# Kernel optimization log

Measured on AMD Instinct MI355X. Metric: run time of the kernel, lower is better.

Reference implementation:

```python
import jax, jax.numpy as jnp
import numpy as np
import math

B, T, C, H = 8, 1024, 1024, 16
D = C // H  # head_size = 64
FF = 4 * C


def setup_inputs() -> dict:
    key = jax.random.key(0)
    ks = jax.random.split(key, 8)
    s = 0.02
    return {
        "x": jax.random.normal(ks[0], (B, T, C), jnp.float32),
        "ln1_g": jnp.ones((C,), jnp.float32),
        "ln1_b": jnp.zeros((C,), jnp.float32),
        "attn_w": jax.random.normal(ks[1], (C, 3 * C), jnp.float32) * s,
        "attn_b": jnp.zeros((3 * C,), jnp.float32),
        "attn_proj_w": jax.random.normal(ks[2], (C, C), jnp.float32) * s,
        "attn_proj_b": jnp.zeros((C,), jnp.float32),
        "ln2_g": jnp.ones((C,), jnp.float32),
        "ln2_b": jnp.zeros((C,), jnp.float32),
        "fc_w": jax.random.normal(ks[3], (C, FF), jnp.float32) * s,
        "fc_b": jnp.zeros((FF,), jnp.float32),
        "mlp_proj_w": jax.random.normal(ks[4], (FF, C), jnp.float32) * s,
        "mlp_proj_b": jnp.zeros((C,), jnp.float32),
    }


def _layernorm(x, g, b, eps=1e-5):
    mu = jnp.mean(x, axis=-1, keepdims=True)
    var = jnp.mean(jnp.square(x - mu), axis=-1, keepdims=True)
    return (x - mu) * jax.lax.rsqrt(var + eps) * g + b


def reference(x, ln1_g, ln1_b, attn_w, attn_b, attn_proj_w, attn_proj_b,
              ln2_g, ln2_b, fc_w, fc_b, mlp_proj_w, mlp_proj_b):
    # --- attention branch (pre-LN) ---
    h = _layernorm(x, ln1_g, ln1_b)
    kqv = h @ attn_w + attn_b                      # (B,T,3C)
    # NOTE: source splits as k, q, v (k first!)
    k, q, v = jnp.split(kqv, 3, axis=-1)
    k = k.reshape(B, T, H, D).transpose(0, 2, 1, 3)  # (B,H,T,D)
    q = q.reshape(B, T, H, D).transpose(0, 2, 1, 3)
    v = v.reshape(B, T, H, D).transpose(0, 2, 1, 3)
    # NOTE: source computes k @ q^T, i.e. wei[i,j] = k_i . q_j
    scale = 1.0 / math.sqrt(D)
    wei = jnp.einsum('bhid,bhjd->bhij', k, q) * scale  # (B,H,T,T)
    causal = jnp.tril(jnp.ones((T, T), dtype=bool))
    wei = jnp.where(causal, wei, -jnp.inf)
    wei = jax.nn.softmax(wei, axis=-1)
    out = jnp.einsum('bhij,bhjd->bhid', wei, v)        # (B,H,T,D)
    out = out.transpose(0, 2, 1, 3).reshape(B, T, C)
    out = out @ attn_proj_w + attn_proj_b
    x = x + out
    # --- MLP branch (pre-LN) ---
    h2 = _layernorm(x, ln2_g, ln2_b)
    m = jax.nn.gelu(h2 @ fc_w + fc_b, approximate=False)  # torch GELU default = exact erf
    m = m @ mlp_proj_w + mlp_proj_b
    return x + m
```

## Files before the change

kernel.cpp:

```cpp
#include <hip/hip_runtime.h>
#include <stdint.h>

typedef unsigned short u16;
typedef __bf16 bf16x8 __attribute__((ext_vector_type(8)));
typedef float f32x4 __attribute__((ext_vector_type(4)));

#define DEVINL static __device__ __forceinline__

DEVINL u16 f2bf(float f) {
  uint32_t u = __builtin_bit_cast(uint32_t, f);
  u += 0x7fffu + ((u >> 16) & 1u);
  return (u16)(u >> 16);
}

DEVINL uint32_t pack_bf2(float f0, float f1) {
  uint32_t u0 = __builtin_bit_cast(uint32_t, f0) + 0x8000u;
  uint32_t u1 = __builtin_bit_cast(uint32_t, f1) + 0x8000u;
  return __builtin_amdgcn_perm(u1, u0, 0x07060302u);
}

DEVINL bf16x8 ld_frag(const u16* p) { return *(const bf16x8*)p; }

DEVINL void gld_lds16(const void* g, void* l) {
  __builtin_amdgcn_global_load_lds((const __attribute__((address_space(1))) void*)g,
                                   (__attribute__((address_space(3))) void*)l, 16, 0, 0);
}

DEVINL int swz4(int r) { return (r & 3) ^ ((r >> 2) & 3); }

DEVINL void xcd_tile(int& tm, int& tn) {
  const int gx = gridDim.x;
  const int flat = blockIdx.x + gx * blockIdx.y;
  const int q = (gx * gridDim.y) >> 3;
  const int wg = (flat & 7) * q + (flat >> 3);
  tn = (wg % gx) * 128;
  tm = (wg / gx) * 128;
}

DEVINL void xcd_tile_wide(int& tm, int& tn) {
  const int gx = gridDim.x;
  const int flat = blockIdx.x + gx * blockIdx.y;
  const int q = (gx * gridDim.y) >> 3;
  const int wg = (flat & 7) * q + (flat >> 3);
  tn = (wg % gx) * 128;
  tm = (wg / gx) * 256;
}

__global__ __launch_bounds__(256)
void transpose_bf16(const float* __restrict__ W, u16* __restrict__ Wt, int K, int N) {
  __shared__ float tile[32][33];
  const int n0 = blockIdx.x * 32, k0 = blockIdx.y * 32;
  const int tx = threadIdx.x, ty = threadIdx.y;
#pragma unroll
  for (int i = 0; i < 32; i += 8)
    tile[ty + i][tx] = W[(size_t)(k0 + ty + i) * N + n0 + tx];
  __syncthreads();
#pragma unroll
  for (int i = 0; i < 32; i += 8)
    Wt[(size_t)(n0 + ty + i) * K + k0 + tx] = f2bf(tile[tx][ty + i]);
}

__global__ __launch_bounds__(256)
void ln_kernel(const float* __restrict__ x, const float* __restrict__ g,
               const float* __restrict__ b, u16* __restrict__ out) {
  __shared__ float red[8];
  const size_t row = blockIdx.x;
  const int tid = threadIdx.x;
  float4 v = ((const float4*)(x + row * 1024))[tid];
  float s = v.x + v.y + v.z + v.w;
  float s2 = v.x * v.x + v.y * v.y + v.z * v.z + v.w * v.w;
#pragma unroll
  for (int o = 32; o; o >>= 1) { s += __shfl_down(s, o); s2 += __shfl_down(s2, o); }
  const int w = tid >> 6;
  if ((tid & 63) == 0) { red[w * 2] = s; red[w * 2 + 1] = s2; }
  __syncthreads();
  const float S = red[0] + red[2] + red[4] + red[6];
  const float S2 = red[1] + red[3] + red[5] + red[7];
  const float mu = S * (1.f / 1024.f);
  const float var = S2 * (1.f / 1024.f) - mu * mu;
  const float rstd = rsqrtf(var + 1e-5f);
  float4 gv = ((const float4*)g)[tid];
  float4 bv = ((const float4*)b)[tid];
  ushort4 o;
  o.x = f2bf((v.x - mu) * rstd * gv.x + bv.x);
  o.y = f2bf((v.y - mu) * rstd * gv.y + bv.y);
  o.z = f2bf((v.z - mu) * rstd * gv.z + bv.z);
  o.w = f2bf((v.w - mu) * rstd * gv.w + bv.w);
  ((ushort4*)(out + row * 1024))[tid] = o;
}

enum { EPI_KQV = 0, EPI_RESID = 1, EPI_GELU = 2, EPI_ADD = 3 };

template <int EPI>
DEVINL void gemm_epilogue(f32x4 (&acc)[4][4], const float* __restrict__ bias,
                          void* __restrict__ outp, const float* __restrict__ resid,
                          int N, int tm, int tn, int mh, int nh, int q4, int c) {
#pragma unroll
  for (int mt = 0; mt < 4; ++mt) {
#pragma unroll
    for (int nt = 0; nt < 4; ++nt) {
      const int col = tn + nh + nt * 16 + c;
      const float bcol = bias[col];
#pragma unroll
      for (int rg = 0; rg < 4; ++rg) {
        const int row = tm + mh + mt * 16 + q4 * 4 + rg;
        float val = acc[mt][nt][rg] + bcol;
        if constexpr (EPI == EPI_KQV) {
          const int bb = row >> 10, t = row & 1023;
          const int s = col >> 10, rem = col & 1023;
          const int hh = rem >> 6, d = rem & 63;
          if (s == 0) val *= 0.18033688011112042f;
          const size_t base = ((size_t)((bb * 16 + hh) * 3 + s)) << 16;
          const size_t idx = (s == 2) ? base + (size_t)d * 1024 + t : base + (size_t)t * 64 + d;
          ((u16*)outp)[idx] = f2bf(val);
        } else if constexpr (EPI == EPI_RESID) {
          const size_t idx = (size_t)row * 1024 + col;
          ((float*)outp)[idx] = val + resid[idx];
        } else if constexpr (EPI == EPI_GELU) {
          const float x2 = val * val;
          const float t = __builtin_fmaf(x2, -0.102952445f, -2.30221235f);
          const float e = __builtin_amdgcn_exp2f(val * t);
          const float ge = val * __builtin_amdgcn_rcpf(1.0f + e);
          ((u16*)outp)[(size_t)row * N + col] = f2bf(ge);
        } else {
          const size_t idx = (size_t)row * 1024 + col;
          ((float*)outp)[idx] += val;
        }
      }
    }
  }
}

template <int EPI>
DEVINL void gemm_body2(const u16* __restrict__ A, const u16* __restrict__ Bt,
                       const float* __restrict__ bias, void* __restrict__ outp,
                       const float* __restrict__ resid, int M, int N, int K,
                       int tm, int tn) {
  __shared__ alignas(16) u16 sA[2][128 * 32];
  __shared__ alignas(16) u16 sB[2][128 * 32];
  const int tid = threadIdx.x;
  const int w = tid >> 6, l = tid & 63;
  const int q4 = l >> 4, c = l & 15;
  const int mh = (w >> 1) * 64, nh = (w & 1) * 64;
  const int cg8 = (q4 ^ swz4(c)) * 8;

  f32x4 acc[4][4] = {};

  const int srow = l >> 2;
  const int scol = ((l & 3) ^ swz4(srow)) * 8;
  const u16* gA0 = A + (size_t)(tm + (w * 2) * 16 + srow) * K + scol;
  const u16* gA1 = A + (size_t)(tm + (w * 2 + 1) * 16 + srow) * K + scol;
  const u16* gB0 = Bt + (size_t)(tn + (w * 2) * 16 + srow) * K + scol;
  const u16* gB1 = Bt + (size_t)(tn + (w * 2 + 1) * 16 + srow) * K + scol;
  const int cA0 = (w * 2) * 512, cA1 = (w * 2 + 1) * 512;

  const int nIters = K / 32;
#define STAGE2(buf, k0)                         \
  do {                                          \
    gld_lds16(gA0 + (k0), &sA[buf][cA0]);       \
    gld_lds16(gA1 + (k0), &sA[buf][cA1]);       \
    gld_lds16(gB0 + (k0), &sB[buf][cA0]);       \
    gld_lds16(gB1 + (k0), &sB[buf][cA1]);       \
  } while (0)

  STAGE2(0, 0);
  for (int i = 0; i < nIters; ++i) {
    const int cur = i & 1;
    asm volatile("s_waitcnt vmcnt(0)" ::: "memory");
    __syncthreads();
    if (i + 1 < nIters) STAGE2(cur ^ 1, (i + 1) * 32);
    const u16* bA = sA[cur];
    const u16* bB = sB[cur];
    bf16x8 af[4], bfv[4];
#pragma unroll
    for (int mt = 0; mt < 4; ++mt) af[mt] = ld_frag(bA + (mh + mt * 16 + c) * 32 + cg8);
#pragma unroll
    for (int nt = 0; nt < 4; ++nt) bfv[nt] = ld_frag(bB + (nh + nt * 16 + c) * 32 + cg8);
#pragma unroll
    for (int mt = 0; mt < 4; ++mt)
#pragma unroll
      for (int nt = 0; nt < 4; ++nt)
        acc[mt][nt] = __builtin_amdgcn_mfma_f32_16x16x32_bf16(af[mt], bfv[nt], acc[mt][nt], 0, 0, 0);
  }
#undef STAGE2
  gemm_epilogue<EPI>(acc, bias, outp, resid, N, tm, tn, mh, nh, q4, c);
}

template <int EPI>
DEVINL void gemm_bodyW(const u16* __restrict__ A, const u16* __restrict__ Bt,
                       const float* __restrict__ bias, void* __restrict__ outp,
                       const float* __restrict__ resid, int N, int K,
                       int tm, int tn) {
  __shared__ alignas(16) u16 sT[3][48 * 512];
  const int tid = threadIdx.x;
  const int w = tid >> 6, l = tid & 63;
  const int q4 = l >> 4, c = l & 15;
  const int mh = (w >> 1) * 64, nh = (w & 1) * 64;

  f32x4 acc[4][4] = {};

  const int lr = l >> 3;
  const int lc = ((l & 7) ^ lr) * 8;
  const u16* gA[4];
  const u16* gB[2];
#pragma unroll
  for (int j = 0; j < 4; ++j) gA[j] = A + (size_t)(tm + 32 * w + j * 8 + lr) * K + lc;
#pragma unroll
  for (int j = 0; j < 2; ++j) gB[j] = Bt + (size_t)(tn + 16 * w + j * 8 + lr) * K + lc;

  auto stageW = [&](int buf, int k0) {
#pragma unroll
    for (int j = 0; j < 4; ++j) gld_lds16(gA[j] + k0, &sT[buf][(4 * w + j) * 512]);
#pragma unroll
    for (int j = 0; j < 2; ++j) gld_lds16(gB[j] + k0, &sT[buf][(32 + 2 * w + j) * 512]);
  };

  auto computeW = [&](int cur) {
    const u16* bufA = sT[cur];
    const u16* bufB = sT[cur] + 32 * 512;
#pragma unroll
    for (int kh = 0; kh < 2; ++kh) {
      bf16x8 af[4], bfv[4];
#pragma unroll
      for (int mt = 0; mt < 4; ++mt) {
        const int row = mh + mt * 16 + c;
        af[mt] = ld_frag(bufA + row * 64 + ((kh * 4 + q4) ^ (c & 7)) * 8);
      }
#pragma unroll
      for (int nt = 0; nt < 4; ++nt) {
        const int row = nh + nt * 16 + c;
        bfv[nt] = ld_frag(bufB + row * 64 + ((kh * 4 + q4) ^ (c & 7)) * 8);
      }
      __builtin_amdgcn_s_setprio(1);
#pragma unroll
      for (int mt = 0; mt < 4; ++mt)
#pragma unroll
        for (int nt = 0; nt < 4; ++nt)
          acc[mt][nt] = __builtin_amdgcn_mfma_f32_16x16x32_bf16(af[mt], bfv[nt], acc[mt][nt], 0, 0, 0);
      __builtin_amdgcn_s_setprio(0);
    }
  };

  const int nI = K / 64;
  stageW(0, 0);
  stageW(1, 64);
  int bc = 0;
  int i = 0;
  for (; i < nI - 1; ++i) {
    asm volatile("s_waitcnt vmcnt(6)" ::: "memory");
    __builtin_amdgcn_s_barrier();
    asm volatile("" ::: "memory");
    if (i + 2 < nI) {
      const int tgt = (bc >= 1) ? bc - 1 : 2;
      stageW(tgt, (i + 2) * 64);
    }
    computeW(bc);
    bc = (bc < 2) ? bc + 1 : 0;
  }
  asm volatile("s_waitcnt vmcnt(0)" ::: "memory");
  __builtin_amdgcn_s_barrier();
  asm volatile("" ::: "memory");
  computeW(bc);

  gemm_epilogue<EPI>(acc, bias, outp, resid, N, tm, tn, mh, nh, q4, c);
}

__global__ __launch_bounds__(256)
void gemm_kqv(const u16* __restrict__ A, const u16* __restrict__ Bt,
              const float* __restrict__ bias, u16* __restrict__ outp,
              int M, int N, int K) {
  int tm, tn;
  xcd_tile(tm, tn);
  gemm_body2<EPI_KQV>(A, Bt, bias, outp, nullptr, M, N, K, tm, tn);
}

__global__ __launch_bounds__(512)
void gemm_gelu(const u16* __restrict__ A, const u16* __restrict__ Bt,
               const float* __restrict__ bias, u16* __restrict__ outp,
               int M, int N, int K) {
  int tm, tn;
  xcd_tile_wide(tm, tn);
  gemm_bodyW<EPI_GELU>(A, Bt, bias, outp, nullptr, N, K, tm, tn);
}

__global__ __launch_bounds__(512)
void gemm_resid(const u16* __restrict__ A, const u16* __restrict__ Bt,
                const float* __restrict__ bias, float* __restrict__ outp,
                const float* __restrict__ resid, int M, int N, int K) {
  int tm, tn;
  xcd_tile_wide(tm, tn);
  gemm_bodyW<EPI_RESID>(A, Bt, bias, outp, resid, N, K, tm, tn);
}

__global__ __launch_bounds__(512)
void gemm_add(const u16* __restrict__ A, const u16* __restrict__ Bt,
              const float* __restrict__ bias, float* __restrict__ outp,
              int M, int N, int K) {
  int tm, tn;
  xcd_tile_wide(tm, tn);
  gemm_bodyW<EPI_ADD>(A, Bt, bias, outp, nullptr, N, K, tm, tn);
}

__global__ __launch_bounds__(256)
void attn_kernel(const u16* __restrict__ kqv, u16* __restrict__ outp) {
  constexpr int LS = 72;
  __shared__ alignas(16) u16 sP[64 * LS];
  __shared__ alignas(16) u16 sK[64 * LS];
  __shared__ alignas(16) u16 sV[64 * LS];
  const int bh = blockIdx.x;
  const int it = (int)gridDim.y - 1 - (int)blockIdx.y;
  const int tid = threadIdx.x;
  const int w = tid >> 6, l = tid & 63, q4 = l >> 4, c = l & 15;
  const int il = w * 16 + c;
  const size_t hb = (size_t)bh * 3 * 65536;
  const u16* qbase = kqv + hb;
  const u16* kbase = kqv + hb + 65536;
  const u16* vbase = kqv + hb + 2 * 65536;

  const int sr = tid >> 3, sc = (tid & 7) * 8;
  const int sr2 = sr + 32;
  *(int4*)&sP[sr * LS + sc] = *(const int4*)(qbase + (size_t)(it * 64 + sr) * 64 + sc);
  *(int4*)&sP[sr2 * LS + sc] = *(const int4*)(qbase + (size_t)(it * 64 + sr2) * 64 + sc);

  f32x4 oacc[4] = {};
  float lsum = 0.f;
  bf16x8 bq0, bq1;

  int4 rk0 = *(const int4*)(kbase + (size_t)sr * 64 + sc);
  int4 rk1 = *(const int4*)(kbase + (size_t)sr2 * 64 + sc);
  int4 rv0 = *(const int4*)(vbase + (size_t)sr * 1024 + sc);
  int4 rv1 = *(const int4*)(vbase + (size_t)sr2 * 1024 + sc);

  for (int jt = 0; jt <= it; ++jt) {
    if (jt) __syncthreads();
    *(int4*)&sK[sr * LS + sc] = rk0;
    *(int4*)&sK[sr2 * LS + sc] = rk1;
    *(int4*)&sV[sr * LS + sc] = rv0;
    *(int4*)&sV[sr2 * LS + sc] = rv1;
    __syncthreads();
    if (jt < it) {
      rk0 = *(const int4*)(kbase + (size_t)((jt + 1) * 64 + sr) * 64 + sc);
      rk1 = *(const int4*)(kbase + (size_t)((jt + 1) * 64 + sr2) * 64 + sc);
      rv0 = *(const int4*)(vbase + (size_t)sr * 1024 + (jt + 1) * 64 + sc);
      rv1 = *(const int4*)(vbase + (size_t)sr2 * 1024 + (jt + 1) * 64 + sc);
    }
    if (jt == 0) {
      bq0 = ld_frag(sP + il * LS + q4 * 8);
      bq1 = ld_frag(sP + il * LS + 32 + q4 * 8);
    }

    f32x4 st[4] = {};
#pragma unroll
    for (int nt = 0; nt < 4; ++nt) {
      st[nt] = __builtin_amdgcn_mfma_f32_16x16x32_bf16(
          ld_frag(sK + (nt * 16 + c) * LS + q4 * 8), bq0, st[nt], 0, 0, 0);
      st[nt] = __builtin_amdgcn_mfma_f32_16x16x32_bf16(
          ld_frag(sK + (nt * 16 + c) * LS + 32 + q4 * 8), bq1, st[nt], 0, 0, 0);
    }

    const bool diag = (jt == it);
    u16* prow = sP + il * LS;
#pragma unroll
    for (int nt = 0; nt < 4; ++nt) {
      float e0 = __builtin_amdgcn_exp2f(st[nt][0]);
      float e1 = __builtin_amdgcn_exp2f(st[nt][1]);
      float e2 = __builtin_amdgcn_exp2f(st[nt][2]);
      float e3 = __builtin_amdgcn_exp2f(st[nt][3]);
      if (diag) {
        const int jb = nt * 16 + q4 * 4;
        e0 = (jb + 0 > il) ? 0.f : e0;
        e1 = (jb + 1 > il) ? 0.f : e1;
        e2 = (jb + 2 > il) ? 0.f : e2;
        e3 = (jb + 3 > il) ? 0.f : e3;
      }
      lsum += (e0 + e1) + (e2 + e3);
      uint2 pk = {pack_bf2(e0, e1), pack_bf2(e2, e3)};
      *(uint2*)&prow[nt * 16 + q4 * 4] = pk;
    }

    bf16x8 bp0 = ld_frag(sP + il * LS + q4 * 8);
    bf16x8 bp1 = ld_frag(sP + il * LS + 32 + q4 * 8);
#pragma unroll
    for (int dt = 0; dt < 4; ++dt) {
      oacc[dt] = __builtin_amdgcn_mfma_f32_16x16x32_bf16(
          ld_frag(sV + (dt * 16 + c) * LS + q4 * 8), bp0, oacc[dt], 0, 0, 0);
      oacc[dt] = __builtin_amdgcn_mfma_f32_16x16x32_bf16(
          ld_frag(sV + (dt * 16 + c) * LS + 32 + q4 * 8), bp1, oacc[dt], 0, 0, 0);
    }
  }

  lsum += __shfl_xor(lsum, 16);
  lsum += __shfl_xor(lsum, 32);
  const float linv = 1.f / lsum;

  const int b_ = bh >> 4, h_ = bh & 15;
  const int t_ = it * 64 + il;
  u16* orow = outp + ((size_t)(b_ * 1024 + t_)) * 1024 + h_ * 64;
#pragma unroll
  for (int dt = 0; dt < 4; ++dt) {
    uint2 ok = {pack_bf2(oacc[dt][0] * linv, oacc[dt][1] * linv),
                pack_bf2(oacc[dt][2] * linv, oacc[dt][3] * linv)};
    *(uint2*)&orow[dt * 16 + q4 * 4] = ok;
  }
}

extern "C" void kernel_launch(void* const* d_in, const int* in_sizes, int n_in,
                              void* d_out, int out_size, void* d_ws, size_t ws_size,
                              hipStream_t stream) {
  const float* x       = (const float*)d_in[0];
  const float* ln1_g   = (const float*)d_in[1];
  const float* ln1_b   = (const float*)d_in[2];
  const float* attn_w  = (const float*)d_in[3];
  const float* attn_b  = (const float*)d_in[4];
  const float* attn_pw = (const float*)d_in[5];
  const float* attn_pb = (const float*)d_in[6];
  const float* ln2_g   = (const float*)d_in[7];
  const float* ln2_b   = (const float*)d_in[8];
  const float* fc_w    = (const float*)d_in[9];
  const float* fc_b    = (const float*)d_in[10];
  const float* mlp_w   = (const float*)d_in[11];
  const float* mlp_b   = (const float*)d_in[12];
  float* out = (float*)d_out;

  u16* ws = (u16*)d_ws;
  u16* mlpT     = ws;
  u16* attn_wT  = mlpT + 1024 * 4096;
  u16* attn_pwT = attn_wT + 3072 * 1024;
  u16* fcT      = attn_pwT + 1024 * 1024;
  u16* hbuf     = fcT + 4096 * 1024;
  u16* kqv      = hbuf + 8192 * 1024;
  u16* attn_o   = kqv + (size_t)8192 * 3072;
  u16* mbuf     = kqv;

  dim3 tb(32, 8);
  transpose_bf16<<<dim3(96, 32),  tb, 0, stream>>>(attn_w,  attn_wT,  1024, 3072);
  transpose_bf16<<<dim3(32, 32),  tb, 0, stream>>>(attn_pw, attn_pwT, 1024, 1024);
  transpose_bf16<<<dim3(128, 32), tb, 0, stream>>>(fc_w,    fcT,      1024, 4096);
  transpose_bf16<<<dim3(32, 128), tb, 0, stream>>>(mlp_w,   mlpT,     4096, 1024);

  ln_kernel<<<8192, 256, 0, stream>>>(x, ln1_g, ln1_b, hbuf);

  gemm_kqv<<<dim3(24, 64), 256, 0, stream>>>(hbuf, attn_wT, attn_b, kqv, 8192, 3072, 1024);

  attn_kernel<<<dim3(128, 16), 256, 0, stream>>>(kqv, attn_o);

  gemm_resid<<<dim3(8, 32), 512, 0, stream>>>(attn_o, attn_pwT, attn_pb, out, x,
                                              8192, 1024, 1024);

  ln_kernel<<<8192, 256, 0, stream>>>(out, ln2_g, ln2_b, hbuf);

  gemm_gelu<<<dim3(32, 32), 512, 0, stream>>>(hbuf, fcT, fc_b, mbuf, 8192, 4096, 1024);

  gemm_add<<<dim3(8, 32), 512, 0, stream>>>(mbuf, mlpT, mlp_b, out, 8192, 1024, 4096);
}
```

Measured before the change: 468.0 us.

## Enlarge attention query tile to 128 rows with 512-thread blocks, drop register prefetch

The attention kernel now handles 128 query rows per block with 8 waves instead of 64 rows with 4 waves, so each loaded K/V tile is shared by twice as many queries. Waves whose rows lie entirely above a key tile skip that tile's compute, and the causal mask uses a per-row threshold. The register double-buffered prefetch of the next K/V tile is removed, so global loads now sit directly between the barriers. The grid is halved, which lowers parallelism and makes per-block work less even across the causal triangle.

```diff
diff --git a/kernel.cpp b/kernel.cpp
--- a/kernel.cpp
+++ b/kernel.cpp
@@ -301,10 +301,10 @@
   gemm_bodyW<EPI_ADD>(A, Bt, bias, outp, nullptr, N, K, tm, tn);
 }
 
-__global__ __launch_bounds__(256)
+__global__ __launch_bounds__(512)
 void attn_kernel(const u16* __restrict__ kqv, u16* __restrict__ outp) {
   constexpr int LS = 72;
-  __shared__ alignas(16) u16 sP[64 * LS];
+  __shared__ alignas(16) u16 sP[128 * LS];
   __shared__ alignas(16) u16 sK[64 * LS];
   __shared__ alignas(16) u16 sV[64 * LS];
   const int bh = blockIdx.x;
@@ -318,36 +318,26 @@
   const u16* vbase = kqv + hb + 2 * 65536;
 
   const int sr = tid >> 3, sc = (tid & 7) * 8;
-  const int sr2 = sr + 32;
-  *(int4*)&sP[sr * LS + sc] = *(const int4*)(qbase + (size_t)(it * 64 + sr) * 64 + sc);
-  *(int4*)&sP[sr2 * LS + sc] = *(const int4*)(qbase + (size_t)(it * 64 + sr2) * 64 + sc);
+  *(int4*)&sP[sr * LS + sc] = *(const int4*)(qbase + (size_t)(it * 128 + sr) * 64 + sc);
+  *(int4*)&sP[(sr + 64) * LS + sc] =
+      *(const int4*)(qbase + (size_t)(it * 128 + sr + 64) * 64 + sc);
 
   f32x4 oacc[4] = {};
   float lsum = 0.f;
   bf16x8 bq0, bq1;
 
-  int4 rk0 = *(const int4*)(kbase + (size_t)sr * 64 + sc);
-  int4 rk1 = *(const int4*)(kbase + (size_t)sr2 * 64 + sc);
-  int4 rv0 = *(const int4*)(vbase + (size_t)sr * 1024 + sc);
-  int4 rv1 = *(const int4*)(vbase + (size_t)sr2 * 1024 + sc);
-
-  for (int jt = 0; jt <= it; ++jt) {
+  const int jtMax = 2 * it + 1;
+  for (int jt = 0; jt <= jtMax; ++jt) {
     if (jt) __syncthreads();
-    *(int4*)&sK[sr * LS + sc] = rk0;
-    *(int4*)&sK[sr2 * LS + sc] = rk1;
-    *(int4*)&sV[sr * LS + sc] = rv0;
-    *(int4*)&sV[sr2 * LS + sc] = rv1;
+    *(int4*)&sK[sr * LS + sc] = *(const int4*)(kbase + (size_t)(jt * 64 + sr) * 64 + sc);
+    *(int4*)&sV[sr * LS + sc] = *(const int4*)(vbase + (size_t)sr * 1024 + jt * 64 + sc);
     __syncthreads();
-    if (jt < it) {
-      rk0 = *(const int4*)(kbase + (size_t)((jt + 1) * 64 + sr) * 64 + sc);
-      rk1 = *(const int4*)(kbase + (size_t)((jt + 1) * 64 + sr2) * 64 + sc);
-      rv0 = *(const int4*)(vbase + (size_t)sr * 1024 + (jt + 1) * 64 + sc);
-      rv1 = *(const int4*)(vbase + (size_t)sr2 * 1024 + (jt + 1) * 64 + sc);
-    }
     if (jt == 0) {
       bq0 = ld_frag(sP + il * LS + q4 * 8);
       bq1 = ld_frag(sP + il * LS + 32 + q4 * 8);
     }
+
+    if (jt * 64 > it * 128 + w * 16 + 15) continue;
 
     f32x4 st[4] = {};
 #pragma unroll
@@ -358,7 +348,8 @@
           ld_frag(sK + (nt * 16 + c) * LS + 32 + q4 * 8), bq1, st[nt], 0, 0, 0);
     }
 
-    const bool diag = (jt == it);
+    const bool diag = (jt >= 2 * it);
+    const int thr = il + it * 128 - jt * 64;
     u16* prow = sP + il * LS;
 #pragma unroll
     for (int nt = 0; nt < 4; ++nt) {
@@ -368,10 +359,10 @@
       float e3 = __builtin_amdgcn_exp2f(st[nt][3]);
       if (diag) {
         const int jb = nt * 16 + q4 * 4;
-        e0 = (jb + 0 > il) ? 0.f : e0;
-        e1 = (jb + 1 > il) ? 0.f : e1;
-        e2 = (jb + 2 > il) ? 0.f : e2;
-        e3 = (jb + 3 > il) ? 0.f : e3;
+        e0 = (jb + 0 > thr) ? 0.f : e0;
+        e1 = (jb + 1 > thr) ? 0.f : e1;
+        e2 = (jb + 2 > thr) ? 0.f : e2;
+        e3 = (jb + 3 > thr) ? 0.f : e3;
       }
       lsum += (e0 + e1) + (e2 + e3);
       uint2 pk = {pack_bf2(e0, e1), pack_bf2(e2, e3)};
@@ -394,7 +385,7 @@
   const float linv = 1.f / lsum;
 
   const int b_ = bh >> 4, h_ = bh & 15;
-  const int t_ = it * 64 + il;
+  const int t_ = it * 128 + il;
   u16* orow = outp + ((size_t)(b_ * 1024 + t_)) * 1024 + h_ * 64;
 #pragma unroll
   for (int dt = 0; dt < 4; ++dt) {
@@ -442,7 +433,7 @@
 
   gemm_kqv<<<dim3(24, 64), 256, 0, stream>>>(hbuf, attn_wT, attn_b, kqv, 8192, 3072, 1024);
 
-  attn_kernel<<<dim3(128, 16), 256, 0, stream>>>(kqv, attn_o);
+  attn_kernel<<<dim3(128, 8), 512, 0, stream>>>(kqv, attn_o);
 
   gemm_resid<<<dim3(8, 32), 512, 0, stream>>>(attn_o, attn_pwT, attn_pb, out, x,
                                               8192, 1024, 1024);
```

After: 451.1 us. 1.04x faster.
